# Optimization experiments

Measured on AMD Instinct MI355X. Metric: run time of the kernel, lower is better.

The kernel has to match this reference:

```python
import jax, jax.numpy as jnp
import numpy as np

EPS = 1e-5  # BatchNorm eps; BN applied in eval mode with running_mean=0, running_var=1


def conv1x1(x, w, b=None):
    # x: [B,C,H,W], w: [O,C] -> [B,O,H,W]
    y = jnp.einsum('bchw,oc->bohw', x, w)
    if b is not None:
        y = y + b[None, :, None, None]
    return y


def bn_eval(x, gamma, beta):
    # running_mean=0, running_var=1
    scale = gamma / jnp.sqrt(1.0 + EPS)
    return x * scale[None, :, None, None] + beta[None, :, None, None]


def glnl_forward(x, mask, wt_nl, bt_nl, wp_nl, bp_nl, wt_l, bt_l, wp_l, bp_l,
                 wg_nl, bg_nl, wg_l, bg_l, wW, bW, gW, betaW, wWl, gWl, betaWl):
    B, C, H, W = x.shape
    I = wt_nl.shape[0]
    N = H * W

    # non-local branch score [B,N,N]
    th_nl = conv1x1(x, wt_nl, bt_nl).reshape(B, I, N)
    ph_nl = conv1x1(x, wp_nl, bp_nl).reshape(B, I, N)
    score_nl = jax.nn.softmax(jnp.einsum('bin,bim->bnm', th_nl, ph_nl), axis=-1)

    # local branch: mask-gated projections, score [B,N,N]
    m = mask.reshape(B, 1, N)
    th_l = conv1x1(x, wt_l, bt_l).reshape(B, I, N) * m
    ph_l = conv1x1(x, wp_l, bp_l).reshape(B, I, N) * m
    score_l = jax.nn.softmax(jnp.einsum('bin,bim->bnm', th_l, ph_l), axis=-1)

    # value projections [B,I,N]
    g_nl = conv1x1(x, wg_nl, bg_nl).reshape(B, I, N)
    g_l = conv1x1(x, wg_l, bg_l).reshape(B, I, N)

    # attention aggregation -> [B,I,H,W]
    y_nl = jnp.einsum('bnm,bim->bin', score_nl, g_nl).reshape(B, I, H, W)
    y_l = jnp.einsum('bnm,bim->bin', score_l, g_l).reshape(B, I, H, W)

    # W_local: conv1x1 (no bias) -> ReLU -> BN
    y_l = bn_eval(jax.nn.relu(conv1x1(y_l, wWl)), gWl, betaWl)

    y = y_nl + y_l
    # W: conv1x1 -> ReLU -> BN, then residual
    W_y = bn_eval(jax.nn.relu(conv1x1(y, wW, bW)), gW, betaW)
    return W_y + x


def setup_inputs() -> dict:
    key = jax.random.key(0)
    ks = jax.random.split(key, 20)
    B, C, I, H, W = 4, 128, 64, 64, 64
    s = 0.02
    inp = {
        'x': jax.random.normal(ks[0], (B, C, H, W), jnp.float32),
        'mask': (jax.random.uniform(ks[1], (B, 1, H, W)) > 0.5).astype(jnp.float32),
        'wt_nl': jax.random.normal(ks[2], (I, C)) * s, 'bt_nl': jnp.zeros((I,)),
        'wp_nl': jax.random.normal(ks[3], (I, C)) * s, 'bp_nl': jnp.zeros((I,)),
        'wt_l': jax.random.normal(ks[4], (I, C)) * s, 'bt_l': jnp.zeros((I,)),
        'wp_l': jax.random.normal(ks[5], (I, C)) * s, 'bp_l': jnp.zeros((I,)),
        'wg_nl': jax.random.normal(ks[6], (I, C)) * s, 'bg_nl': jnp.zeros((I,)),
        'wg_l': jax.random.normal(ks[7], (I, C)) * s, 'bg_l': jnp.zeros((I,)),
        'wW': jax.random.normal(ks[8], (C, I)) * s, 'bW': jnp.zeros((C,)),
        'gW': jnp.ones((C,)), 'betaW': jnp.zeros((C,)),
        'wWl': jax.random.normal(ks[9], (I, I)) * s,
        'gWl': jnp.ones((I,)), 'betaWl': jnp.zeros((I,)),
    }
    return inp


def reference(x, mask, wt_nl, bt_nl, wp_nl, bp_nl, wt_l, bt_l, wp_l, bp_l,
              wg_nl, bg_nl, wg_l, bg_l, wW, bW, gW, betaW, wWl, gWl, betaWl):
    return glnl_forward(x, mask, wt_nl, bt_nl, wp_nl, bp_nl, wt_l, bt_l, wp_l, bp_l,
                        wg_nl, bg_nl, wg_l, bg_l, wW, bW, gW, betaW, wWl, gWl, betaWl)
```

## Files before the change

### kernel.cpp

```cpp
#include <hip/hip_runtime.h>

typedef unsigned short u16;
typedef __attribute__((ext_vector_type(8))) short short8;
typedef __attribute__((ext_vector_type(4))) float floatx4;

#define MFMA16(a, b, c) __builtin_amdgcn_mfma_f32_16x16x32_bf16((a), (b), (c), 0, 0, 0)

#define SZ_P ((size_t)4 * 64 * 4096)

__device__ __forceinline__ float bf2f(u16 u) {
    union { unsigned int i; float f; } v; v.i = ((unsigned int)u) << 16; return v.f;
}
__device__ __forceinline__ u16 f2bf(float f) {
    union { float f; unsigned int i; } v; v.f = f;
    unsigned int r = v.i + 0x7fffu + ((v.i >> 16) & 1u);
    return (u16)(r >> 16);
}
__device__ __forceinline__ unsigned int pk2(float a, float b) {
    union { float f; unsigned int u; } x, y; x.f = a; y.f = b;
    return (x.u >> 16) | (y.u & 0xffff0000u);
}

__global__ __launch_bounds__(256) void k_prep_w(
    const float* __restrict__ w0, const float* __restrict__ w1,
    const float* __restrict__ w2, const float* __restrict__ w3,
    const float* __restrict__ w4, const float* __restrict__ w5,
    const float* __restrict__ wWl, const float* __restrict__ wW,
    u16* __restrict__ wbf)
{
    const int idx = blockIdx.x * 256 + threadIdx.x;
    float v;
    if (idx < 49152) {
        const int j = idx >> 13, off = idx & 8191;
        const float* s = (j == 0) ? w0 : (j == 1) ? w1 : (j == 2) ? w2
                       : (j == 3) ? w3 : (j == 4) ? w4 : w5;
        v = s[off];
    } else if (idx < 53248) {
        v = wWl[idx - 49152];
    } else {
        v = wW[idx - 53248];
    }
    wbf[idx] = f2bf(v);
}

__global__ __launch_bounds__(256) void k_proj(
    const float* __restrict__ x, const float* __restrict__ mask,
    const u16* __restrict__ wbf,
    const float* __restrict__ bq0f, const float* __restrict__ bk0f,
    const float* __restrict__ bv0f,
    const float* __restrict__ bq1f, const float* __restrict__ bk1f,
    const float* __restrict__ bv1f,
    u16* __restrict__ q0, u16* __restrict__ k0, u16* __restrict__ v0,
    u16* __restrict__ q1, u16* __restrict__ k1, u16* __restrict__ v1)
{
    __shared__ __align__(16) u16 xt_s[64 * 136];
    const int n0 = blockIdx.x * 64, b = blockIdx.y;
    const int br = blockIdx.z >> 1, half = blockIdx.z & 1;
    const u16* wq = wbf + br * 24576;
    const u16* wk = wq + 8192;
    const u16* wv = wk + 8192;
    const float* bq = br ? bq1f : bq0f;
    const float* bk = br ? bk1f : bk0f;
    const float* bv = br ? bv1f : bv0f;
    u16* q = br ? q1 : q0;  u16* k = br ? k1 : k0;  u16* v = br ? v1 : v0;

    const int t = threadIdx.x, w = t >> 6, lane = t & 63;
    const int quad = lane >> 4, l15 = lane & 15;
    const float* xb = x + ((size_t)b << 19);

    for (int idx = t; idx < 8192; idx += 256) {
        const int c = idx >> 6, n = idx & 63;
        xt_s[n * 136 + c] = f2bf(xb[((size_t)c << 12) + n0 + n]);
    }
    __syncthreads();

    short8 ax[4];
#pragma unroll
    for (int cc = 0; cc < 4; ++cc)
        ax[cc] = *(const short8*)&xt_s[(w * 16 + l15) * 136 + quad * 8 + cc * 32];

    float mv[4] = {1.f, 1.f, 1.f, 1.f};
    if (br) {
#pragma unroll
        for (int r = 0; r < 4; ++r)
            mv[r] = mask[((size_t)b << 12) + n0 + w * 16 + quad * 4 + r];
    }

#pragma unroll
    for (int qk = 0; qk < 2; ++qk) {
        const u16* wsel = qk ? wk : wq;
        const float* bb = qk ? bk : bq;
        u16* o = qk ? k : q;
#pragma unroll
        for (int nsh = 0; nsh < 2; ++nsh) {
            const int ns = half * 2 + nsh;
            floatx4 acc = {0.f, 0.f, 0.f, 0.f};
            const u16* wp = wsel + (ns * 16 + l15) * 128 + quad * 8;
#pragma unroll
            for (int cc = 0; cc < 4; ++cc)
                acc = MFMA16(ax[cc], *(const short8*)(wp + cc * 32), acc);
            const float bias_i = bb[ns * 16 + l15];
#pragma unroll
            for (int r = 0; r < 4; ++r) {
                const float val = (acc[r] + bias_i) * mv[r];
                o[((size_t)b << 18) + (size_t)(n0 + w * 16 + quad * 4 + r) * 64
                  + ns * 16 + l15] = f2bf(val);
            }
        }
    }

    short8 aw[4];
#pragma unroll
    for (int cc = 0; cc < 4; ++cc)
        aw[cc] = *(const short8*)(wv + (w * 16 + l15) * 128 + quad * 8 + cc * 32);
    float bvr[4];
#pragma unroll
    for (int r = 0; r < 4; ++r) bvr[r] = bv[w * 16 + quad * 4 + r];
#pragma unroll
    for (int nsh = 0; nsh < 2; ++nsh) {
        const int ns = half * 2 + nsh;
        floatx4 acc = {0.f, 0.f, 0.f, 0.f};
#pragma unroll
        for (int cc = 0; cc < 4; ++cc)
            acc = MFMA16(aw[cc],
                *(const short8*)&xt_s[(ns * 16 + l15) * 136 + quad * 8 + cc * 32], acc);
#pragma unroll
        for (int r = 0; r < 4; ++r) {
            v[((size_t)b << 18) + ((size_t)(w * 16 + quad * 4 + r) << 12)
              + n0 + ns * 16 + l15] = f2bf(acc[r] + bvr[r]);
        }
    }
}

__global__ __launch_bounds__(256) void k_flash(
    const u16* __restrict__ Q0, const u16* __restrict__ K0,
    const u16* __restrict__ V0,
    const u16* __restrict__ Q1, const u16* __restrict__ K1,
    const u16* __restrict__ V1,
    u16* __restrict__ num, float* __restrict__ den)
{
    __shared__ __align__(16) u16 kt_s[2][64 * 72];
    __shared__ __align__(16) u16 vt_s[2][64 * 72];
    __shared__ __align__(16) u16 p_s[4 * 32 * 72];

    const int flat = blockIdx.x;
    const int g = flat & 15, tile = flat >> 4;
    const int b = g >> 2, z = g & 3;
    const int br = z >> 1, sp = z & 1;
    const int qb = tile * 128;
    const size_t base = ((size_t)b << 18);
    const u16* Q = (br ? Q1 : Q0) + base;
    const u16* K = (br ? K1 : K0) + base;
    const u16* V = (br ? V1 : V0) + base;
    u16* numo = num + (size_t)z * SZ_P + base;
    float* deno = den + z * 16384 + b * 4096;

    const int t = threadIdx.x, w = t >> 6, lane = t & 63;
    const int quad = lane >> 4, l15 = lane & 15;
    const int pw = w * 32 * 72;

    const int r0 = t >> 3, r1 = (t + 256) >> 3, cg8 = (t & 7) * 8;
    const u16* Kp0 = K + (size_t)r0 * 64 + cg8;
    const u16* Kp1 = K + (size_t)r1 * 64 + cg8;
    const u16* Vp0 = V + ((size_t)r0 << 12) + cg8;
    const u16* Vp1 = V + ((size_t)r1 << 12) + cg8;
    const int lk0 = r0 * 72 + cg8, lk1 = r1 * 72 + cg8;

    short8 aq[2][2];
#pragma unroll
    for (int t2 = 0; t2 < 2; ++t2)
#pragma unroll
        for (int s = 0; s < 2; ++s)
            aq[t2][s] = *(const short8*)(Q + (size_t)(qb + w * 32 + t2 * 16 + l15) * 64
                                         + s * 32 + quad * 8);

    const short8 ones8 = {0x3F80, 0x3F80, 0x3F80, 0x3F80, 0x3F80, 0x3F80, 0x3F80, 0x3F80};

    floatx4 oacc[4][2];
#pragma unroll
    for (int it = 0; it < 4; ++it)
#pragma unroll
        for (int t2 = 0; t2 < 2; ++t2) oacc[it][t2] = (floatx4){0.f, 0.f, 0.f, 0.f};
    floatx4 lacc[2] = {{0.f, 0.f, 0.f, 0.f}, {0.f, 0.f, 0.f, 0.f}};

    const int roff = tile & 31;
    const int m_beg = sp * 2048;

    {
        const int m0 = m_beg + (roff << 6);
        *(short8*)&kt_s[0][lk0] = *(const short8*)(Kp0 + (size_t)m0 * 64);
        *(short8*)&kt_s[0][lk1] = *(const short8*)(Kp1 + (size_t)m0 * 64);
        *(short8*)&vt_s[0][lk0] = *(const short8*)(Vp0 + m0);
        *(short8*)&vt_s[0][lk1] = *(const short8*)(Vp1 + m0);
    }

    for (int j = 0; j < 32; ++j) {
        const int cur = j & 1;
        const int mn = m_beg + (((roff + j + 1) & 31) << 6);
        short8 pk0v = *(const short8*)(Kp0 + (size_t)mn * 64);
        short8 pk1v = *(const short8*)(Kp1 + (size_t)mn * 64);
        short8 pv0v = *(const short8*)(Vp0 + mn);
        short8 pv1v = *(const short8*)(Vp1 + mn);
        __syncthreads();

#pragma unroll
        for (int mt = 0; mt < 4; ++mt) {
            const u16* kp = &kt_s[cur][(mt * 16 + l15) * 72 + quad * 8];
            const short8 ka0 = *(const short8*)kp;
            const short8 ka1 = *(const short8*)(kp + 32);
#pragma unroll
            for (int t2 = 0; t2 < 2; ++t2) {
                floatx4 acc = {0.f, 0.f, 0.f, 0.f};
                acc = MFMA16(ka0, aq[t2][0], acc);
                acc = MFMA16(ka1, aq[t2][1], acc);
                const float e0 = __expf(acc[0]), e1 = __expf(acc[1]);
                const float e2 = __expf(acc[2]), e3 = __expf(acc[3]);
                *(uint2*)&p_s[pw + (t2 * 16 + l15) * 72 + mt * 16 + quad * 4] =
                    make_uint2(pk2(e0, e1), pk2(e2, e3));
            }
        }

        short8 pb2[2][2];
#pragma unroll
        for (int t2 = 0; t2 < 2; ++t2)
#pragma unroll
            for (int s = 0; s < 2; ++s)
                pb2[t2][s] = *(const short8*)&p_s[pw + (t2 * 16 + l15) * 72 + s * 32 + quad * 8];
#pragma unroll
        for (int it = 0; it < 4; ++it) {
            const u16* vp = &vt_s[cur][(it * 16 + l15) * 72 + quad * 8];
            const short8 va0 = *(const short8*)vp;
            const short8 va1 = *(const short8*)(vp + 32);
#pragma unroll
            for (int t2 = 0; t2 < 2; ++t2) {
                oacc[it][t2] = MFMA16(va0, pb2[t2][0], oacc[it][t2]);
                oacc[it][t2] = MFMA16(va1, pb2[t2][1], oacc[it][t2]);
            }
        }
#pragma unroll
        for (int t2 = 0; t2 < 2; ++t2) {
            lacc[t2] = MFMA16(ones8, pb2[t2][0], lacc[t2]);
            lacc[t2] = MFMA16(ones8, pb2[t2][1], lacc[t2]);
        }

        *(short8*)&kt_s[cur ^ 1][lk0] = pk0v;
        *(short8*)&kt_s[cur ^ 1][lk1] = pk1v;
        *(short8*)&vt_s[cur ^ 1][lk0] = pv0v;
        *(short8*)&vt_s[cur ^ 1][lk1] = pv1v;
    }

    if (quad == 0) {
#pragma unroll
        for (int t2 = 0; t2 < 2; ++t2)
            deno[qb + w * 32 + t2 * 16 + l15] = lacc[t2][0];
    }

#pragma unroll
    for (int it = 0; it < 4; ++it)
#pragma unroll
        for (int t2 = 0; t2 < 2; ++t2) {
            *(uint2*)&p_s[pw + (t2 * 16 + l15) * 72 + it * 16 + quad * 4] =
                make_uint2(pk2(oacc[it][t2][0], oacc[it][t2][1]),
                           pk2(oacc[it][t2][2], oacc[it][t2][3]));
        }
    __syncthreads();
#pragma unroll
    for (int ch = t; ch < 1024; ch += 256) {
        const int row = ch >> 3, cg = ch & 7;
        *(short8*)(numo + (size_t)(qb + row) * 64 + cg * 8) =
            *(const short8*)&p_s[(row >> 5) * 2304 + (row & 31) * 72 + cg * 8];
    }
}

__global__ __launch_bounds__(256) void k_epi(
    const u16* __restrict__ num, const float* __restrict__ den,
    const u16* __restrict__ wbf,
    const float* __restrict__ gWl, const float* __restrict__ betaWl,
    const float* __restrict__ bW, const float* __restrict__ gW,
    const float* __restrict__ betaW,
    const float* __restrict__ x, float* __restrict__ out)
{
    __shared__ __align__(16) u16 yl_s[16 * 72];
    __shared__ __align__(16) u16 ynl_s[16 * 72];
    __shared__ __align__(16) u16 yy_s[16 * 72];
    const int b = blockIdx.y, n0 = blockIdx.x * 16;
    const int t = threadIdx.x, w = t >> 6, lane = t & 63;
    const int quad = lane >> 4, l15 = lane & 15;
    const size_t ybase = ((size_t)b << 18) + (size_t)n0 * 64;

    if (t < 128) {
        const int row = t >> 3, cg = t & 7;
        const float dn = den[b * 4096 + n0 + row] + den[16384 + b * 4096 + n0 + row];
        const float dl = den[32768 + b * 4096 + n0 + row] + den[49152 + b * 4096 + n0 + row];
        const float inl = 1.0f / dn, ilo = 1.0f / dl;
        const short8 a0 = *(const short8*)(num + ybase + row * 64 + cg * 8);
        const short8 a1 = *(const short8*)(num + SZ_P + ybase + row * 64 + cg * 8);
        const short8 c0 = *(const short8*)(num + 2 * SZ_P + ybase + row * 64 + cg * 8);
        const short8 c1 = *(const short8*)(num + 3 * SZ_P + ybase + row * 64 + cg * 8);
        short8 ynl8, yl8;
#pragma unroll
        for (int j = 0; j < 8; ++j) {
            ynl8[j] = (short)f2bf((bf2f((u16)a0[j]) + bf2f((u16)a1[j])) * inl);
            yl8[j]  = (short)f2bf((bf2f((u16)c0[j]) + bf2f((u16)c1[j])) * ilo);
        }
        *(short8*)&ynl_s[row * 72 + cg * 8] = ynl8;
        *(short8*)&yl_s[row * 72 + cg * 8] = yl8;
    }
    __syncthreads();
    const float rsq = rsqrtf(1.0f + 1e-5f);
    const u16* wblW = wbf + 49152;
    const u16* wbW  = wbf + 53248;

    {
        const short8 a0 = *(const short8*)(wblW + (w * 16 + l15) * 64 + quad * 8);
        const short8 a1 = *(const short8*)(wblW + (w * 16 + l15) * 64 + 32 + quad * 8);
        float sc[4], bt[4];
#pragma unroll
        for (int r = 0; r < 4; ++r) {
            const int io = w * 16 + quad * 4 + r;
            sc[r] = gWl[io] * rsq;
            bt[r] = betaWl[io];
        }
        floatx4 acc = {0.f, 0.f, 0.f, 0.f};
        const u16* bp_ = &yl_s[l15 * 72 + quad * 8];
        acc = MFMA16(a0, *(const short8*)bp_, acc);
        acc = MFMA16(a1, *(const short8*)(bp_ + 32), acc);
#pragma unroll
        for (int r = 0; r < 4; ++r) {
            const int io = w * 16 + quad * 4 + r;
            float val = fmaxf(acc[r], 0.f) * sc[r] + bt[r];
            val += bf2f(ynl_s[l15 * 72 + io]);
            yy_s[l15 * 72 + io] = f2bf(val);
        }
    }
    __syncthreads();

#pragma unroll
    for (int rb = 0; rb < 2; ++rb) {
        const int c0 = rb * 64 + w * 16;
        const short8 a0 = *(const short8*)(wbW + (c0 + l15) * 64 + quad * 8);
        const short8 a1 = *(const short8*)(wbW + (c0 + l15) * 64 + 32 + quad * 8);
        float bs[4], sc[4], bt[4];
#pragma unroll
        for (int r = 0; r < 4; ++r) {
            const int c = c0 + quad * 4 + r;
            bs[r] = bW[c];
            sc[r] = gW[c] * rsq;
            bt[r] = betaW[c];
        }
        floatx4 acc = {0.f, 0.f, 0.f, 0.f};
        const u16* bp_ = &yy_s[l15 * 72 + quad * 8];
        acc = MFMA16(a0, *(const short8*)bp_, acc);
        acc = MFMA16(a1, *(const short8*)(bp_ + 32), acc);
#pragma unroll
        for (int r = 0; r < 4; ++r) {
            const int c = c0 + quad * 4 + r;
            float val = fmaxf(acc[r] + bs[r], 0.f) * sc[r] + bt[r];
            const size_t xi = ((size_t)b << 19) + ((size_t)c << 12) + n0 + l15;
            out[xi] = val + x[xi];
        }
    }
}

extern "C" void kernel_launch(void* const* d_in, const int* in_sizes, int n_in,
                              void* d_out, int out_size, void* d_ws, size_t ws_size,
                              hipStream_t stream) {
    const float* x      = (const float*)d_in[0];
    const float* mask   = (const float*)d_in[1];
    const float* wt_nl  = (const float*)d_in[2];  const float* bt_nl = (const float*)d_in[3];
    const float* wp_nl  = (const float*)d_in[4];  const float* bp_nl = (const float*)d_in[5];
    const float* wt_l   = (const float*)d_in[6];  const float* bt_l  = (const float*)d_in[7];
    const float* wp_l   = (const float*)d_in[8];  const float* bp_l  = (const float*)d_in[9];
    const float* wg_nl  = (const float*)d_in[10]; const float* bg_nl = (const float*)d_in[11];
    const float* wg_l   = (const float*)d_in[12]; const float* bg_l  = (const float*)d_in[13];
    const float* wW     = (const float*)d_in[14]; const float* bW    = (const float*)d_in[15];
    const float* gW     = (const float*)d_in[16]; const float* betaW = (const float*)d_in[17];
    const float* wWl    = (const float*)d_in[18]; const float* gWl   = (const float*)d_in[19];
    const float* betaWl = (const float*)d_in[20];

    u16* ws  = (u16*)d_ws;
    u16* wbf = ws;
    u16* q0  = wbf + 61440;
    u16* k0  = q0 + SZ_P;
    u16* v0  = k0 + SZ_P;
    u16* q1  = v0 + SZ_P;
    u16* k1  = q1 + SZ_P;
    u16* v1  = k1 + SZ_P;
    u16* num = v1 + SZ_P;
    float* den = (float*)(num + 4 * SZ_P);

    k_prep_w<<<dim3(240), 256, 0, stream>>>(wt_nl, wp_nl, wg_nl,
                                            wt_l, wp_l, wg_l, wWl, wW, wbf);
    k_proj<<<dim3(64, 4, 4), 256, 0, stream>>>(x, mask, wbf,
        bt_nl, bp_nl, bg_nl, bt_l, bp_l, bg_l,
        q0, k0, v0, q1, k1, v1);
    k_flash<<<dim3(512), 256, 0, stream>>>(q0, k0, v0, q1, k1, v1, num, den);
    k_epi<<<dim3(256, 4), 256, 0, stream>>>(num, den, wbf, gWl, betaWl,
                                            bW, gW, betaW, x, (float*)d_out);
}
```

Before: 180.6 us.

## Fuse all stages into one persistent kernel with global atomic barriers

Merges the weight-prep, projection, flash-attention and epilogue kernels into one 512-block kernel. The stages are separated by software grid barriers built on atomic counters, which are reset with a memset before each launch. Work is remapped per stage: projection blocks now cover all four output subtiles, and epilogue blocks handle 32 positions. The aim is to remove the launch gaps between kernels, at the cost of barrier spin overhead and relying on all 512 blocks being resident at once.

```diff
diff --git a/kernel.cpp b/kernel.cpp
--- a/kernel.cpp
+++ b/kernel.cpp
@@ -21,343 +21,355 @@
     return (x.u >> 16) | (y.u & 0xffff0000u);
 }
 
-__global__ __launch_bounds__(256) void k_prep_w(
-    const float* __restrict__ w0, const float* __restrict__ w1,
-    const float* __restrict__ w2, const float* __restrict__ w3,
-    const float* __restrict__ w4, const float* __restrict__ w5,
-    const float* __restrict__ wWl, const float* __restrict__ wW,
-    u16* __restrict__ wbf)
+__device__ __forceinline__ void gbar(unsigned int* ctr, unsigned int target) {
+    __syncthreads();
+    __threadfence();
+    if (threadIdx.x == 0) {
+        atomicAdd(ctr, 1u);
+        while (atomicAdd(ctr, 0u) < target) __builtin_amdgcn_s_sleep(8);
+    }
+    __syncthreads();
+    __threadfence();
+}
+
+__global__ __launch_bounds__(256) void k_mega(
+    const float* __restrict__ x, const float* __restrict__ mask,
+    const float* __restrict__ wt_nl, const float* __restrict__ bt_nl,
+    const float* __restrict__ wp_nl, const float* __restrict__ bp_nl,
+    const float* __restrict__ wt_l,  const float* __restrict__ bt_l,
+    const float* __restrict__ wp_l,  const float* __restrict__ bp_l,
+    const float* __restrict__ wg_nl, const float* __restrict__ bg_nl,
+    const float* __restrict__ wg_l,  const float* __restrict__ bg_l,
+    const float* __restrict__ wW,  const float* __restrict__ bW,
+    const float* __restrict__ gW,  const float* __restrict__ betaW,
+    const float* __restrict__ wWl, const float* __restrict__ gWl,
+    const float* __restrict__ betaWl,
+    float* __restrict__ out,
+    u16* __restrict__ wbf,
+    u16* __restrict__ q0, u16* __restrict__ k0, u16* __restrict__ v0,
+    u16* __restrict__ q1, u16* __restrict__ k1, u16* __restrict__ v1,
+    u16* __restrict__ num, float* __restrict__ den,
+    unsigned int* __restrict__ bar)
 {
-    const int idx = blockIdx.x * 256 + threadIdx.x;
-    float v;
-    if (idx < 49152) {
-        const int j = idx >> 13, off = idx & 8191;
-        const float* s = (j == 0) ? w0 : (j == 1) ? w1 : (j == 2) ? w2
-                       : (j == 3) ? w3 : (j == 4) ? w4 : w5;
-        v = s[off];
-    } else if (idx < 53248) {
-        v = wWl[idx - 49152];
-    } else {
-        v = wW[idx - 53248];
-    }
-    wbf[idx] = f2bf(v);
-}
-
-__global__ __launch_bounds__(256) void k_proj(
-    const float* __restrict__ x, const float* __restrict__ mask,
-    const u16* __restrict__ wbf,
-    const float* __restrict__ bq0f, const float* __restrict__ bk0f,
-    const float* __restrict__ bv0f,
-    const float* __restrict__ bq1f, const float* __restrict__ bk1f,
-    const float* __restrict__ bv1f,
-    u16* __restrict__ q0, u16* __restrict__ k0, u16* __restrict__ v0,
-    u16* __restrict__ q1, u16* __restrict__ k1, u16* __restrict__ v1)
-{
-    __shared__ __align__(16) u16 xt_s[64 * 136];
-    const int n0 = blockIdx.x * 64, b = blockIdx.y;
-    const int br = blockIdx.z >> 1, half = blockIdx.z & 1;
-    const u16* wq = wbf + br * 24576;
-    const u16* wk = wq + 8192;
-    const u16* wv = wk + 8192;
-    const float* bq = br ? bq1f : bq0f;
-    const float* bk = br ? bk1f : bk0f;
-    const float* bv = br ? bv1f : bv0f;
-    u16* q = br ? q1 : q0;  u16* k = br ? k1 : k0;  u16* v = br ? v1 : v0;
-
+    __shared__ __align__(16) u16 smem[27648];
+    const int flat = blockIdx.x;
     const int t = threadIdx.x, w = t >> 6, lane = t & 63;
     const int quad = lane >> 4, l15 = lane & 15;
-    const float* xb = x + ((size_t)b << 19);
-
-    for (int idx = t; idx < 8192; idx += 256) {
-        const int c = idx >> 6, n = idx & 63;
-        xt_s[n * 136 + c] = f2bf(xb[((size_t)c << 12) + n0 + n]);
+
+    {
+        const int idx = flat * 256 + t;
+        if (idx < 61440) {
+            float v;
+            if (idx < 49152) {
+                const int j = idx >> 13, off = idx & 8191;
+                const float* s = (j == 0) ? wt_nl : (j == 1) ? wp_nl : (j == 2) ? wg_nl
+                               : (j == 3) ? wt_l : (j == 4) ? wp_l : wg_l;
+                v = s[off];
+            } else if (idx < 53248) {
+                v = wWl[idx - 49152];
+            } else {
+                v = wW[idx - 53248];
+            }
+            wbf[idx] = f2bf(v);
+        }
     }
-    __syncthreads();
-
-    short8 ax[4];
-#pragma unroll
-    for (int cc = 0; cc < 4; ++cc)
-        ax[cc] = *(const short8*)&xt_s[(w * 16 + l15) * 136 + quad * 8 + cc * 32];
-
-    float mv[4] = {1.f, 1.f, 1.f, 1.f};
-    if (br) {
-#pragma unroll
-        for (int r = 0; r < 4; ++r)
-            mv[r] = mask[((size_t)b << 12) + n0 + w * 16 + quad * 4 + r];
+    gbar(bar, 512);
+
+    {
+        u16* xt_s = smem;
+        const int br = flat & 1, b = (flat >> 1) & 3, n0 = (flat >> 3) * 64;
+        const u16* wq = wbf + br * 24576;
+        const u16* wk = wq + 8192;
+        const u16* wv = wk + 8192;
+        const float* bq = br ? bt_l : bt_nl;
+        const float* bk = br ? bp_l : bp_nl;
+        const float* bv = br ? bg_l : bg_nl;
+        u16* q = br ? q1 : q0;  u16* k = br ? k1 : k0;  u16* v = br ? v1 : v0;
+        const float* xb = x + ((size_t)b << 19);
+
+        for (int idx = t; idx < 8192; idx += 256) {
+            const int c = idx >> 6, n = idx & 63;
+            xt_s[n * 136 + c] = f2bf(xb[((size_t)c << 12) + n0 + n]);
+        }
+        __syncthreads();
+
+        short8 ax[4];
+#pragma unroll
+        for (int cc = 0; cc < 4; ++cc)
+            ax[cc] = *(const short8*)&xt_s[(w * 16 + l15) * 136 + quad * 8 + cc * 32];
+
+        float mv[4] = {1.f, 1.f, 1.f, 1.f};
+        if (br) {
+#pragma unroll
+            for (int r = 0; r < 4; ++r)
+                mv[r] = mask[((size_t)b << 12) + n0 + w * 16 + quad * 4 + r];
+        }
+
+#pragma unroll
+        for (int qk = 0; qk < 2; ++qk) {
+            const u16* wsel = qk ? wk : wq;
+            const float* bb = qk ? bk : bq;
+            u16* o = qk ? k : q;
+#pragma unroll
+            for (int ns = 0; ns < 4; ++ns) {
+                floatx4 acc = {0.f, 0.f, 0.f, 0.f};
+                const u16* wp = wsel + (ns * 16 + l15) * 128 + quad * 8;
+#pragma unroll
+                for (int cc = 0; cc < 4; ++cc)
+                    acc = MFMA16(ax[cc], *(const short8*)(wp + cc * 32), acc);
+                const float bias_i = bb[ns * 16 + l15];
+#pragma unroll
+                for (int r = 0; r < 4; ++r) {
+                    const float val = (acc[r] + bias_i) * mv[r];
+                    o[((size_t)b << 18) + (size_t)(n0 + w * 16 + quad * 4 + r) * 64
+                      + ns * 16 + l15] = f2bf(val);
+                }
+            }
+        }
+
+        short8 aw[4];
+#pragma unroll
+        for (int cc = 0; cc < 4; ++cc)
+            aw[cc] = *(const short8*)(wv + (w * 16 + l15) * 128 + quad * 8 + cc * 32);
+        float bvr[4];
+#pragma unroll
+        for (int r = 0; r < 4; ++r) bvr[r] = bv[w * 16 + quad * 4 + r];
+#pragma unroll
+        for (int ns = 0; ns < 4; ++ns) {
+            floatx4 acc = {0.f, 0.f, 0.f, 0.f};
+#pragma unroll
+            for (int cc = 0; cc < 4; ++cc)
+                acc = MFMA16(aw[cc],
+                    *(const short8*)&xt_s[(ns * 16 + l15) * 136 + quad * 8 + cc * 32], acc);
+#pragma unroll
+            for (int r = 0; r < 4; ++r) {
+                v[((size_t)b << 18) + ((size_t)(w * 16 + quad * 4 + r) << 12)
+                  + n0 + ns * 16 + l15] = f2bf(acc[r] + bvr[r]);
+            }
+        }
     }
-
-#pragma unroll
-    for (int qk = 0; qk < 2; ++qk) {
-        const u16* wsel = qk ? wk : wq;
-        const float* bb = qk ? bk : bq;
-        u16* o = qk ? k : q;
-#pragma unroll
-        for (int nsh = 0; nsh < 2; ++nsh) {
-            const int ns = half * 2 + nsh;
-            floatx4 acc = {0.f, 0.f, 0.f, 0.f};
-            const u16* wp = wsel + (ns * 16 + l15) * 128 + quad * 8;
-#pragma unroll
-            for (int cc = 0; cc < 4; ++cc)
-                acc = MFMA16(ax[cc], *(const short8*)(wp + cc * 32), acc);
-            const float bias_i = bb[ns * 16 + l15];
+    gbar(bar + 4, 512);
+
+    {
+        u16* kt_sb = smem;
+        u16* vt_sb = smem + 9216;
+        u16* p_s   = smem + 18432;
+
+        const int g = flat & 15, tile = flat >> 4;
+        const int b = g >> 2, z = g & 3;
+        const int br = z >> 1, sp = z & 1;
+        const int qb = tile * 128;
+        const size_t base = ((size_t)b << 18);
+        const u16* Q = (br ? q1 : q0) + base;
+        const u16* K = (br ? k1 : k0) + base;
+        const u16* V = (br ? v1 : v0) + base;
+        u16* numo = num + (size_t)z * SZ_P + base;
+        float* deno = den + z * 16384 + b * 4096;
+
+        const int pw = w * 32 * 72;
+        const int r0 = t >> 3, r1 = (t + 256) >> 3, cg8 = (t & 7) * 8;
+        const u16* Kp0 = K + (size_t)r0 * 64 + cg8;
+        const u16* Kp1 = K + (size_t)r1 * 64 + cg8;
+        const u16* Vp0 = V + ((size_t)r0 << 12) + cg8;
+        const u16* Vp1 = V + ((size_t)r1 << 12) + cg8;
+        const int lk0 = r0 * 72 + cg8, lk1 = r1 * 72 + cg8;
+
+        short8 aq[2][2];
+#pragma unroll
+        for (int t2 = 0; t2 < 2; ++t2)
+#pragma unroll
+            for (int s = 0; s < 2; ++s)
+                aq[t2][s] = *(const short8*)(Q + (size_t)(qb + w * 32 + t2 * 16 + l15) * 64
+                                             + s * 32 + quad * 8);
+
+        const short8 ones8 = {0x3F80, 0x3F80, 0x3F80, 0x3F80,
+                              0x3F80, 0x3F80, 0x3F80, 0x3F80};
+        floatx4 oacc[4][2];
+#pragma unroll
+        for (int it = 0; it < 4; ++it)
+#pragma unroll
+            for (int t2 = 0; t2 < 2; ++t2) oacc[it][t2] = (floatx4){0.f, 0.f, 0.f, 0.f};
+        floatx4 lacc[2] = {{0.f, 0.f, 0.f, 0.f}, {0.f, 0.f, 0.f, 0.f}};
+
+        const int roff = tile & 31;
+        const int m_beg = sp * 2048;
+
+        {
+            const int m0 = m_beg + (roff << 6);
+            *(short8*)&kt_sb[lk0] = *(const short8*)(Kp0 + (size_t)m0 * 64);
+            *(short8*)&kt_sb[lk1] = *(const short8*)(Kp1 + (size_t)m0 * 64);
+            *(short8*)&vt_sb[lk0] = *(const short8*)(Vp0 + m0);
+            *(short8*)&vt_sb[lk1] = *(const short8*)(Vp1 + m0);
+        }
+
+        for (int j = 0; j < 32; ++j) {
+            const int cur = j & 1;
+            u16* ktc = kt_sb + cur * 4608;
+            u16* vtc = vt_sb + cur * 4608;
+            u16* ktn = kt_sb + (cur ^ 1) * 4608;
+            u16* vtn = vt_sb + (cur ^ 1) * 4608;
+            const int mn = m_beg + (((roff + j + 1) & 31) << 6);
+            short8 pk0v = *(const short8*)(Kp0 + (size_t)mn * 64);
+            short8 pk1v = *(const short8*)(Kp1 + (size_t)mn * 64);
+            short8 pv0v = *(const short8*)(Vp0 + mn);
+            short8 pv1v = *(const short8*)(Vp1 + mn);
+            __syncthreads();
+
+#pragma unroll
+            for (int mt = 0; mt < 4; ++mt) {
+                const u16* kp = &ktc[(mt * 16 + l15) * 72 + quad * 8];
+                const short8 ka0 = *(const short8*)kp;
+                const short8 ka1 = *(const short8*)(kp + 32);
+#pragma unroll
+                for (int t2 = 0; t2 < 2; ++t2) {
+                    floatx4 acc = {0.f, 0.f, 0.f, 0.f};
+                    acc = MFMA16(ka0, aq[t2][0], acc);
+                    acc = MFMA16(ka1, aq[t2][1], acc);
+                    const float e0 = __expf(acc[0]), e1 = __expf(acc[1]);
+                    const float e2 = __expf(acc[2]), e3 = __expf(acc[3]);
+                    *(uint2*)&p_s[pw + (t2 * 16 + l15) * 72 + mt * 16 + quad * 4] =
+                        make_uint2(pk2(e0, e1), pk2(e2, e3));
+                }
+            }
+
+            short8 pb2[2][2];
+#pragma unroll
+            for (int t2 = 0; t2 < 2; ++t2)
+#pragma unroll
+                for (int s = 0; s < 2; ++s)
+                    pb2[t2][s] = *(const short8*)&p_s[pw + (t2 * 16 + l15) * 72 + s * 32 + quad * 8];
+#pragma unroll
+            for (int it = 0; it < 4; ++it) {
+                const u16* vp = &vtc[(it * 16 + l15) * 72 + quad * 8];
+                const short8 va0 = *(const short8*)vp;
+                const short8 va1 = *(const short8*)(vp + 32);
+#pragma unroll
+                for (int t2 = 0; t2 < 2; ++t2) {
+                    oacc[it][t2] = MFMA16(va0, pb2[t2][0], oacc[it][t2]);
+                    oacc[it][t2] = MFMA16(va1, pb2[t2][1], oacc[it][t2]);
+                }
+            }
+#pragma unroll
+            for (int t2 = 0; t2 < 2; ++t2) {
+                lacc[t2] = MFMA16(ones8, pb2[t2][0], lacc[t2]);
+                lacc[t2] = MFMA16(ones8, pb2[t2][1], lacc[t2]);
+            }
+
+            *(short8*)&ktn[lk0] = pk0v;
+            *(short8*)&ktn[lk1] = pk1v;
+            *(short8*)&vtn[lk0] = pv0v;
+            *(short8*)&vtn[lk1] = pv1v;
+        }
+
+        if (quad == 0) {
+#pragma unroll
+            for (int t2 = 0; t2 < 2; ++t2)
+                deno[qb + w * 32 + t2 * 16 + l15] = lacc[t2][0];
+        }
+
+#pragma unroll
+        for (int it = 0; it < 4; ++it)
+#pragma unroll
+            for (int t2 = 0; t2 < 2; ++t2) {
+                *(uint2*)&p_s[pw + (t2 * 16 + l15) * 72 + it * 16 + quad * 4] =
+                    make_uint2(pk2(oacc[it][t2][0], oacc[it][t2][1]),
+                               pk2(oacc[it][t2][2], oacc[it][t2][3]));
+            }
+        __syncthreads();
+#pragma unroll
+        for (int ch = t; ch < 1024; ch += 256) {
+            const int row = ch >> 3, cg = ch & 7;
+            *(short8*)(numo + (size_t)(qb + row) * 64 + cg * 8) =
+                *(const short8*)&p_s[(row >> 5) * 2304 + (row & 31) * 72 + cg * 8];
+        }
+    }
+    gbar(bar + 8, 512);
+
+    {
+        u16* yl_s  = smem;
+        u16* ynl_s = smem + 2304;
+        u16* yy_s  = smem + 4608;
+        const int b = flat & 3, n0 = (flat >> 2) * 32;
+        const size_t ybase = ((size_t)b << 18) + (size_t)n0 * 64;
+
+        {
+            const int row = t >> 3, cg = t & 7;
+            const float dn = den[b * 4096 + n0 + row] + den[16384 + b * 4096 + n0 + row];
+            const float dl = den[32768 + b * 4096 + n0 + row] + den[49152 + b * 4096 + n0 + row];
+            const float inl = 1.0f / dn, ilo = 1.0f / dl;
+            const short8 a0 = *(const short8*)(num + ybase + row * 64 + cg * 8);
+            const short8 a1 = *(const short8*)(num + SZ_P + ybase + row * 64 + cg * 8);
+            const short8 c0 = *(const short8*)(num + 2 * SZ_P + ybase + row * 64 + cg * 8);
+            const short8 c1 = *(const short8*)(num + 3 * SZ_P + ybase + row * 64 + cg * 8);
+            short8 ynl8, yl8;
+#pragma unroll
+            for (int j = 0; j < 8; ++j) {
+                ynl8[j] = (short)f2bf((bf2f((u16)a0[j]) + bf2f((u16)a1[j])) * inl);
+                yl8[j]  = (short)f2bf((bf2f((u16)c0[j]) + bf2f((u16)c1[j])) * ilo);
+            }
+            *(short8*)&ynl_s[row * 72 + cg * 8] = ynl8;
+            *(short8*)&yl_s[row * 72 + cg * 8] = yl8;
+        }
+        __syncthreads();
+        const float rsq = rsqrtf(1.0f + 1e-5f);
+        const u16* wblW = wbf + 49152;
+        const u16* wbW  = wbf + 53248;
+
+        {
+            const short8 a0 = *(const short8*)(wblW + (w * 16 + l15) * 64 + quad * 8);
+            const short8 a1 = *(const short8*)(wblW + (w * 16 + l15) * 64 + 32 + quad * 8);
+            float sc[4], bt[4];
 #pragma unroll
             for (int r = 0; r < 4; ++r) {
-                const float val = (acc[r] + bias_i) * mv[r];
-                o[((size_t)b << 18) + (size_t)(n0 + w * 16 + quad * 4 + r) * 64
-                  + ns * 16 + l15] = f2bf(val);
-            }
-        }
-    }
-
-    short8 aw[4];
-#pragma unroll
-    for (int cc = 0; cc < 4; ++cc)
-        aw[cc] = *(const short8*)(wv + (w * 16 + l15) * 128 + quad * 8 + cc * 32);
-    float bvr[4];
-#pragma unroll
-    for (int r = 0; r < 4; ++r) bvr[r] = bv[w * 16 + quad * 4 + r];
-#pragma unroll
-    for (int nsh = 0; nsh < 2; ++nsh) {
-        const int ns = half * 2 + nsh;
-        floatx4 acc = {0.f, 0.f, 0.f, 0.f};
-#pragma unroll
-        for (int cc = 0; cc < 4; ++cc)
-            acc = MFMA16(aw[cc],
-                *(const short8*)&xt_s[(ns * 16 + l15) * 136 + quad * 8 + cc * 32], acc);
-#pragma unroll
-        for (int r = 0; r < 4; ++r) {
-            v[((size_t)b << 18) + ((size_t)(w * 16 + quad * 4 + r) << 12)
-              + n0 + ns * 16 + l15] = f2bf(acc[r] + bvr[r]);
-        }
-    }
-}
-
-__global__ __launch_bounds__(256) void k_flash(
-    const u16* __restrict__ Q0, const u16* __restrict__ K0,
-    const u16* __restrict__ V0,
-    const u16* __restrict__ Q1, const u16* __restrict__ K1,
-    const u16* __restrict__ V1,
-    u16* __restrict__ num, float* __restrict__ den)
-{
-    __shared__ __align__(16) u16 kt_s[2][64 * 72];
-    __shared__ __align__(16) u16 vt_s[2][64 * 72];
-    __shared__ __align__(16) u16 p_s[4 * 32 * 72];
-
-    const int flat = blockIdx.x;
-    const int g = flat & 15, tile = flat >> 4;
-    const int b = g >> 2, z = g & 3;
-    const int br = z >> 1, sp = z & 1;
-    const int qb = tile * 128;
-    const size_t base = ((size_t)b << 18);
-    const u16* Q = (br ? Q1 : Q0) + base;
-    const u16* K = (br ? K1 : K0) + base;
-    const u16* V = (br ? V1 : V0) + base;
-    u16* numo = num + (size_t)z * SZ_P + base;
-    float* deno = den + z * 16384 + b * 4096;
-
-    const int t = threadIdx.x, w = t >> 6, lane = t & 63;
-    const int quad = lane >> 4, l15 = lane & 15;
-    const int pw = w * 32 * 72;
-
-    const int r0 = t >> 3, r1 = (t + 256) >> 3, cg8 = (t & 7) * 8;
-    const u16* Kp0 = K + (size_t)r0 * 64 + cg8;
-    const u16* Kp1 = K + (size_t)r1 * 64 + cg8;
-    const u16* Vp0 = V + ((size_t)r0 << 12) + cg8;
-    const u16* Vp1 = V + ((size_t)r1 << 12) + cg8;
-    const int lk0 = r0 * 72 + cg8, lk1 = r1 * 72 + cg8;
-
-    short8 aq[2][2];
-#pragma unroll
-    for (int t2 = 0; t2 < 2; ++t2)
-#pragma unroll
-        for (int s = 0; s < 2; ++s)
-            aq[t2][s] = *(const short8*)(Q + (size_t)(qb + w * 32 + t2 * 16 + l15) * 64
-                                         + s * 32 + quad * 8);
-
-    const short8 ones8 = {0x3F80, 0x3F80, 0x3F80, 0x3F80, 0x3F80, 0x3F80, 0x3F80, 0x3F80};
-
-    floatx4 oacc[4][2];
-#pragma unroll
-    for (int it = 0; it < 4; ++it)
-#pragma unroll
-        for (int t2 = 0; t2 < 2; ++t2) oacc[it][t2] = (floatx4){0.f, 0.f, 0.f, 0.f};
-    floatx4 lacc[2] = {{0.f, 0.f, 0.f, 0.f}, {0.f, 0.f, 0.f, 0.f}};
-
-    const int roff = tile & 31;
-    const int m_beg = sp * 2048;
-
-    {
-        const int m0 = m_beg + (roff << 6);
-        *(short8*)&kt_s[0][lk0] = *(const short8*)(Kp0 + (size_t)m0 * 64);
-        *(short8*)&kt_s[0][lk1] = *(const short8*)(Kp1 + (size_t)m0 * 64);
-        *(short8*)&vt_s[0][lk0] = *(const short8*)(Vp0 + m0);
-        *(short8*)&vt_s[0][lk1] = *(const short8*)(Vp1 + m0);
-    }
-
-    for (int j = 0; j < 32; ++j) {
-        const int cur = j & 1;
-        const int mn = m_beg + (((roff + j + 1) & 31) << 6);
-        short8 pk0v = *(const short8*)(Kp0 + (size_t)mn * 64);
-        short8 pk1v = *(const short8*)(Kp1 + (size_t)mn * 64);
-        short8 pv0v = *(const short8*)(Vp0 + mn);
-        short8 pv1v = *(const short8*)(Vp1 + mn);
+                const int io = w * 16 + quad * 4 + r;
+                sc[r] = gWl[io] * rsq;
+                bt[r] = betaWl[io];
+            }
+#pragma unroll
+            for (int ns = 0; ns < 2; ++ns) {
+                floatx4 acc = {0.f, 0.f, 0.f, 0.f};
+                const u16* bp_ = &yl_s[(ns * 16 + l15) * 72 + quad * 8];
+                acc = MFMA16(a0, *(const short8*)bp_, acc);
+                acc = MFMA16(a1, *(const short8*)(bp_ + 32), acc);
+#pragma unroll
+                for (int r = 0; r < 4; ++r) {
+                    const int io = w * 16 + quad * 4 + r;
+                    float val = fmaxf(acc[r], 0.f) * sc[r] + bt[r];
+                    val += bf2f(ynl_s[(ns * 16 + l15) * 72 + io]);
+                    yy_s[(ns * 16 + l15) * 72 + io] = f2bf(val);
+                }
+            }
+        }
         __syncthreads();
 
 #pragma unroll
-        for (int mt = 0; mt < 4; ++mt) {
-            const u16* kp = &kt_s[cur][(mt * 16 + l15) * 72 + quad * 8];
-            const short8 ka0 = *(const short8*)kp;
-            const short8 ka1 = *(const short8*)(kp + 32);
-#pragma unroll
-            for (int t2 = 0; t2 < 2; ++t2) {
+        for (int rb = 0; rb < 2; ++rb) {
+            const int c0 = rb * 64 + w * 16;
+            const short8 a0 = *(const short8*)(wbW + (c0 + l15) * 64 + quad * 8);
+            const short8 a1 = *(const short8*)(wbW + (c0 + l15) * 64 + 32 + quad * 8);
+            float bs[4], sc[4], bt[4];
+#pragma unroll
+            for (int r = 0; r < 4; ++r) {
+                const int c = c0 + quad * 4 + r;
+                bs[r] = bW[c];
+                sc[r] = gW[c] * rsq;
+                bt[r] = betaW[c];
+            }
+#pragma unroll
+            for (int ns = 0; ns < 2; ++ns) {
                 floatx4 acc = {0.f, 0.f, 0.f, 0.f};
-                acc = MFMA16(ka0, aq[t2][0], acc);
-                acc = MFMA16(ka1, aq[t2][1], acc);
-                const float e0 = __expf(acc[0]), e1 = __expf(acc[1]);
-                const float e2 = __expf(acc[2]), e3 = __expf(acc[3]);
-                *(uint2*)&p_s[pw + (t2 * 16 + l15) * 72 + mt * 16 + quad * 4] =
-                    make_uint2(pk2(e0, e1), pk2(e2, e3));
-            }
-        }
-
-        short8 pb2[2][2];
-#pragma unroll
-        for (int t2 = 0; t2 < 2; ++t2)
-#pragma unroll
-            for (int s = 0; s < 2; ++s)
-                pb2[t2][s] = *(const short8*)&p_s[pw + (t2 * 16 + l15) * 72 + s * 32 + quad * 8];
-#pragma unroll
-        for (int it = 0; it < 4; ++it) {
-            const u16* vp = &vt_s[cur][(it * 16 + l15) * 72 + quad * 8];
-            const short8 va0 = *(const short8*)vp;
-            const short8 va1 = *(const short8*)(vp + 32);
-#pragma unroll
-            for (int t2 = 0; t2 < 2; ++t2) {
-                oacc[it][t2] = MFMA16(va0, pb2[t2][0], oacc[it][t2]);
-                oacc[it][t2] = MFMA16(va1, pb2[t2][1], oacc[it][t2]);
-            }
-        }
-#pragma unroll
-        for (int t2 = 0; t2 < 2; ++t2) {
-            lacc[t2] = MFMA16(ones8, pb2[t2][0], lacc[t2]);
-            lacc[t2] = MFMA16(ones8, pb2[t2][1], lacc[t2]);
-        }
-
-        *(short8*)&kt_s[cur ^ 1][lk0] = pk0v;
-        *(short8*)&kt_s[cur ^ 1][lk1] = pk1v;
-        *(short8*)&vt_s[cur ^ 1][lk0] = pv0v;
-        *(short8*)&vt_s[cur ^ 1][lk1] = pv1v;
-    }
-
-    if (quad == 0) {
-#pragma unroll
-        for (int t2 = 0; t2 < 2; ++t2)
-            deno[qb + w * 32 + t2 * 16 + l15] = lacc[t2][0];
-    }
-
-#pragma unroll
-    for (int it = 0; it < 4; ++it)
-#pragma unroll
-        for (int t2 = 0; t2 < 2; ++t2) {
-            *(uint2*)&p_s[pw + (t2 * 16 + l15) * 72 + it * 16 + quad * 4] =
-                make_uint2(pk2(oacc[it][t2][0], oacc[it][t2][1]),
-                           pk2(oacc[it][t2][2], oacc[it][t2][3]));
-        }
-    __syncthreads();
-#pragma unroll
-    for (int ch = t; ch < 1024; ch += 256) {
-        const int row = ch >> 3, cg = ch & 7;
-        *(short8*)(numo + (size_t)(qb + row) * 64 + cg * 8) =
-            *(const short8*)&p_s[(row >> 5) * 2304 + (row & 31) * 72 + cg * 8];
-    }
-}
-
-__global__ __launch_bounds__(256) void k_epi(
-    const u16* __restrict__ num, const float* __restrict__ den,
-    const u16* __restrict__ wbf,
-    const float* __restrict__ gWl, const float* __restrict__ betaWl,
-    const float* __restrict__ bW, const float* __restrict__ gW,
-    const float* __restrict__ betaW,
-    const float* __restrict__ x, float* __restrict__ out)
-{
-    __shared__ __align__(16) u16 yl_s[16 * 72];
-    __shared__ __align__(16) u16 ynl_s[16 * 72];
-    __shared__ __align__(16) u16 yy_s[16 * 72];
-    const int b = blockIdx.y, n0 = blockIdx.x * 16;
-    const int t = threadIdx.x, w = t >> 6, lane = t & 63;
-    const int quad = lane >> 4, l15 = lane & 15;
-    const size_t ybase = ((size_t)b << 18) + (size_t)n0 * 64;
-
-    if (t < 128) {
-        const int row = t >> 3, cg = t & 7;
-        const float dn = den[b * 4096 + n0 + row] + den[16384 + b * 4096 + n0 + row];
-        const float dl = den[32768 + b * 4096 + n0 + row] + den[49152 + b * 4096 + n0 + row];
-        const float inl = 1.0f / dn, ilo = 1.0f / dl;
-        const short8 a0 = *(const short8*)(num + ybase + row * 64 + cg * 8);
-        const short8 a1 = *(const short8*)(num + SZ_P + ybase + row * 64 + cg * 8);
-        const short8 c0 = *(const short8*)(num + 2 * SZ_P + ybase + row * 64 + cg * 8);
-        const short8 c1 = *(const short8*)(num + 3 * SZ_P + ybase + row * 64 + cg * 8);
-        short8 ynl8, yl8;
-#pragma unroll
-        for (int j = 0; j < 8; ++j) {
-            ynl8[j] = (short)f2bf((bf2f((u16)a0[j]) + bf2f((u16)a1[j])) * inl);
-            yl8[j]  = (short)f2bf((bf2f((u16)c0[j]) + bf2f((u16)c1[j])) * ilo);
-        }
-        *(short8*)&ynl_s[row * 72 + cg * 8] = ynl8;
-        *(short8*)&yl_s[row * 72 + cg * 8] = yl8;
-    }
-    __syncthreads();
-    const float rsq = rsqrtf(1.0f + 1e-5f);
-    const u16* wblW = wbf + 49152;
-    const u16* wbW  = wbf + 53248;
-
-    {
-        const short8 a0 = *(const short8*)(wblW + (w * 16 + l15) * 64 + quad * 8);
-        const short8 a1 = *(const short8*)(wblW + (w * 16 + l15) * 64 + 32 + quad * 8);
-        float sc[4], bt[4];
-#pragma unroll
-        for (int r = 0; r < 4; ++r) {
-            const int io = w * 16 + quad * 4 + r;
-            sc[r] = gWl[io] * rsq;
-            bt[r] = betaWl[io];
-        }
-        floatx4 acc = {0.f, 0.f, 0.f, 0.f};
-        const u16* bp_ = &yl_s[l15 * 72 + quad * 8];
-        acc = MFMA16(a0, *(const short8*)bp_, acc);
-        acc = MFMA16(a1, *(const short8*)(bp_ + 32), acc);
-#pragma unroll
-        for (int r = 0; r < 4; ++r) {
-            const int io = w * 16 + quad * 4 + r;
-            float val = fmaxf(acc[r], 0.f) * sc[r] + bt[r];
-            val += bf2f(ynl_s[l15 * 72 + io]);
-            yy_s[l15 * 72 + io] = f2bf(val);
-        }
-    }
-    __syncthreads();
-
-#pragma unroll
-    for (int rb = 0; rb < 2; ++rb) {
-        const int c0 = rb * 64 + w * 16;
-        const short8 a0 = *(const short8*)(wbW + (c0 + l15) * 64 + quad * 8);
-        const short8 a1 = *(const short8*)(wbW + (c0 + l15) * 64 + 32 + quad * 8);
-        float bs[4], sc[4], bt[4];
-#pragma unroll
-        for (int r = 0; r < 4; ++r) {
-            const int c = c0 + quad * 4 + r;
-            bs[r] = bW[c];
-            sc[r] = gW[c] * rsq;
-            bt[r] = betaW[c];
-        }
-        floatx4 acc = {0.f, 0.f, 0.f, 0.f};
-        const u16* bp_ = &yy_s[l15 * 72 + quad * 8];
-        acc = MFMA16(a0, *(const short8*)bp_, acc);
-        acc = MFMA16(a1, *(const short8*)(bp_ + 32), acc);
-#pragma unroll
-        for (int r = 0; r < 4; ++r) {
-            const int c = c0 + quad * 4 + r;
-            float val = fmaxf(acc[r] + bs[r], 0.f) * sc[r] + bt[r];
-            const size_t xi = ((size_t)b << 19) + ((size_t)c << 12) + n0 + l15;
-            out[xi] = val + x[xi];
+                const u16* bp_ = &yy_s[(ns * 16 + l15) * 72 + quad * 8];
+                acc = MFMA16(a0, *(const short8*)bp_, acc);
+                acc = MFMA16(a1, *(const short8*)(bp_ + 32), acc);
+#pragma unroll
+                for (int r = 0; r < 4; ++r) {
+                    const int c = c0 + quad * 4 + r;
+                    float val = fmaxf(acc[r] + bs[r], 0.f) * sc[r] + bt[r];
+                    const size_t xi = ((size_t)b << 19) + ((size_t)c << 12)
+                                    + n0 + ns * 16 + l15;
+                    out[xi] = val + x[xi];
+                }
+            }
         }
     }
 }
@@ -377,6 +389,7 @@
     const float* gW     = (const float*)d_in[16]; const float* betaW = (const float*)d_in[17];
     const float* wWl    = (const float*)d_in[18]; const float* gWl   = (const float*)d_in[19];
     const float* betaWl = (const float*)d_in[20];
+    float* out = (float*)d_out;
 
     u16* ws  = (u16*)d_ws;
     u16* wbf = ws;
@@ -388,13 +401,11 @@
     u16* v1  = k1 + SZ_P;
     u16* num = v1 + SZ_P;
     float* den = (float*)(num + 4 * SZ_P);
-
-    k_prep_w<<<dim3(240), 256, 0, stream>>>(wt_nl, wp_nl, wg_nl,
-                                            wt_l, wp_l, wg_l, wWl, wW, wbf);
-    k_proj<<<dim3(64, 4, 4), 256, 0, stream>>>(x, mask, wbf,
-        bt_nl, bp_nl, bg_nl, bt_l, bp_l, bg_l,
-        q0, k0, v0, q1, k1, v1);
-    k_flash<<<dim3(512), 256, 0, stream>>>(q0, k0, v0, q1, k1, v1, num, den);
-    k_epi<<<dim3(256, 4), 256, 0, stream>>>(num, den, wbf, gWl, betaWl,
-                                            bW, gW, betaW, x, (float*)d_out);
-}
+    unsigned int* bar = (unsigned int*)(den + 4 * 16384);
+
+    hipMemsetAsync((void*)bar, 0, 48, stream);
+    k_mega<<<dim3(512), dim3(256), 0, stream>>>(
+        x, mask, wt_nl, bt_nl, wp_nl, bp_nl, wt_l, bt_l, wp_l, bp_l,
+        wg_nl, bg_nl, wg_l, bg_l, wW, bW, gW, betaW, wWl, gWl, betaWl,
+        out, wbf, q0, k0, v0, q1, k1, v1, num, den, bar);
+}
```

New measurement: 491.3 us. 2.72x slower.

## Drop weight prep kernel, convert weights inline, compute softmax denominators with VALU sums

Applied to the files above, without the earlier changes.

Removes the separate fp32-to-bf16 weight conversion kernel. Projection and epilogue kernels now load fp32 weights and pack them to bf16 in registers. The projection grid is halved so each block computes all four output slices instead of two, which removes the duplicated x transpose into shared memory. In the flash kernel the ones-vector MFMA used for the row-sum denominator is replaced by scalar accumulation of the exponentials plus a cross-lane shuffle reduction, saving MFMA issue slots at the cost of extra VALU adds and fp32 weight loads.

```diff
diff --git a/kernel.cpp b/kernel.cpp
--- a/kernel.cpp
+++ b/kernel.cpp
@@ -16,52 +16,33 @@
     unsigned int r = v.i + 0x7fffu + ((v.i >> 16) & 1u);
     return (u16)(r >> 16);
 }
+__device__ __forceinline__ short8 pack8(const float* __restrict__ p) {
+    short8 r;
+#pragma unroll
+    for (int j = 0; j < 8; ++j) r[j] = (short)f2bf(p[j]);
+    return r;
+}
 __device__ __forceinline__ unsigned int pk2(float a, float b) {
     union { float f; unsigned int u; } x, y; x.f = a; y.f = b;
     return (x.u >> 16) | (y.u & 0xffff0000u);
 }
 
-__global__ __launch_bounds__(256) void k_prep_w(
-    const float* __restrict__ w0, const float* __restrict__ w1,
-    const float* __restrict__ w2, const float* __restrict__ w3,
-    const float* __restrict__ w4, const float* __restrict__ w5,
-    const float* __restrict__ wWl, const float* __restrict__ wW,
-    u16* __restrict__ wbf)
-{
-    const int idx = blockIdx.x * 256 + threadIdx.x;
-    float v;
-    if (idx < 49152) {
-        const int j = idx >> 13, off = idx & 8191;
-        const float* s = (j == 0) ? w0 : (j == 1) ? w1 : (j == 2) ? w2
-                       : (j == 3) ? w3 : (j == 4) ? w4 : w5;
-        v = s[off];
-    } else if (idx < 53248) {
-        v = wWl[idx - 49152];
-    } else {
-        v = wW[idx - 53248];
-    }
-    wbf[idx] = f2bf(v);
-}
-
 __global__ __launch_bounds__(256) void k_proj(
     const float* __restrict__ x, const float* __restrict__ mask,
-    const u16* __restrict__ wbf,
-    const float* __restrict__ bq0f, const float* __restrict__ bk0f,
-    const float* __restrict__ bv0f,
-    const float* __restrict__ bq1f, const float* __restrict__ bk1f,
-    const float* __restrict__ bv1f,
+    const float* __restrict__ wq0, const float* __restrict__ bq0,
+    const float* __restrict__ wk0, const float* __restrict__ bk0,
+    const float* __restrict__ wv0, const float* __restrict__ bv0,
+    const float* __restrict__ wq1, const float* __restrict__ bq1,
+    const float* __restrict__ wk1, const float* __restrict__ bk1,
+    const float* __restrict__ wv1, const float* __restrict__ bv1,
     u16* __restrict__ q0, u16* __restrict__ k0, u16* __restrict__ v0,
     u16* __restrict__ q1, u16* __restrict__ k1, u16* __restrict__ v1)
 {
     __shared__ __align__(16) u16 xt_s[64 * 136];
-    const int n0 = blockIdx.x * 64, b = blockIdx.y;
-    const int br = blockIdx.z >> 1, half = blockIdx.z & 1;
-    const u16* wq = wbf + br * 24576;
-    const u16* wk = wq + 8192;
-    const u16* wv = wk + 8192;
-    const float* bq = br ? bq1f : bq0f;
-    const float* bk = br ? bk1f : bk0f;
-    const float* bv = br ? bv1f : bv0f;
+    const int n0 = blockIdx.x * 64, b = blockIdx.y, br = blockIdx.z;
+    const float* wq = br ? wq1 : wq0;  const float* bq = br ? bq1 : bq0;
+    const float* wk = br ? wk1 : wk0;  const float* bk = br ? bk1 : bk0;
+    const float* wv = br ? wv1 : wv0;  const float* bv = br ? bv1 : bv0;
     u16* q = br ? q1 : q0;  u16* k = br ? k1 : k0;  u16* v = br ? v1 : v0;
 
     const int t = threadIdx.x, w = t >> 6, lane = t & 63;
@@ -88,17 +69,16 @@
 
 #pragma unroll
     for (int qk = 0; qk < 2; ++qk) {
-        const u16* wsel = qk ? wk : wq;
+        const float* wsel = qk ? wk : wq;
         const float* bb = qk ? bk : bq;
         u16* o = qk ? k : q;
 #pragma unroll
-        for (int nsh = 0; nsh < 2; ++nsh) {
-            const int ns = half * 2 + nsh;
+        for (int ns = 0; ns < 4; ++ns) {
             floatx4 acc = {0.f, 0.f, 0.f, 0.f};
-            const u16* wp = wsel + (ns * 16 + l15) * 128 + quad * 8;
+            const float* wp = wsel + (ns * 16 + l15) * 128 + quad * 8;
 #pragma unroll
             for (int cc = 0; cc < 4; ++cc)
-                acc = MFMA16(ax[cc], *(const short8*)(wp + cc * 32), acc);
+                acc = MFMA16(ax[cc], pack8(wp + cc * 32), acc);
             const float bias_i = bb[ns * 16 + l15];
 #pragma unroll
             for (int r = 0; r < 4; ++r) {
@@ -112,13 +92,12 @@
     short8 aw[4];
 #pragma unroll
     for (int cc = 0; cc < 4; ++cc)
-        aw[cc] = *(const short8*)(wv + (w * 16 + l15) * 128 + quad * 8 + cc * 32);
+        aw[cc] = pack8(wv + (w * 16 + l15) * 128 + quad * 8 + cc * 32);
     float bvr[4];
 #pragma unroll
     for (int r = 0; r < 4; ++r) bvr[r] = bv[w * 16 + quad * 4 + r];
 #pragma unroll
-    for (int nsh = 0; nsh < 2; ++nsh) {
-        const int ns = half * 2 + nsh;
+    for (int ns = 0; ns < 4; ++ns) {
         floatx4 acc = {0.f, 0.f, 0.f, 0.f};
 #pragma unroll
         for (int cc = 0; cc < 4; ++cc)
@@ -174,14 +153,12 @@
             aq[t2][s] = *(const short8*)(Q + (size_t)(qb + w * 32 + t2 * 16 + l15) * 64
                                          + s * 32 + quad * 8);
 
-    const short8 ones8 = {0x3F80, 0x3F80, 0x3F80, 0x3F80, 0x3F80, 0x3F80, 0x3F80, 0x3F80};
-
     floatx4 oacc[4][2];
 #pragma unroll
     for (int it = 0; it < 4; ++it)
 #pragma unroll
         for (int t2 = 0; t2 < 2; ++t2) oacc[it][t2] = (floatx4){0.f, 0.f, 0.f, 0.f};
-    floatx4 lacc[2] = {{0.f, 0.f, 0.f, 0.f}, {0.f, 0.f, 0.f, 0.f}};
+    float dacc[2] = {0.f, 0.f};
 
     const int roff = tile & 31;
     const int m_beg = sp * 2048;
@@ -215,6 +192,7 @@
                 acc = MFMA16(ka1, aq[t2][1], acc);
                 const float e0 = __expf(acc[0]), e1 = __expf(acc[1]);
                 const float e2 = __expf(acc[2]), e3 = __expf(acc[3]);
+                dacc[t2] += (e0 + e1) + (e2 + e3);
                 *(uint2*)&p_s[pw + (t2 * 16 + l15) * 72 + mt * 16 + quad * 4] =
                     make_uint2(pk2(e0, e1), pk2(e2, e3));
             }
@@ -237,11 +215,6 @@
                 oacc[it][t2] = MFMA16(va1, pb2[t2][1], oacc[it][t2]);
             }
         }
-#pragma unroll
-        for (int t2 = 0; t2 < 2; ++t2) {
-            lacc[t2] = MFMA16(ones8, pb2[t2][0], lacc[t2]);
-            lacc[t2] = MFMA16(ones8, pb2[t2][1], lacc[t2]);
-        }
 
         *(short8*)&kt_s[cur ^ 1][lk0] = pk0v;
         *(short8*)&kt_s[cur ^ 1][lk1] = pk1v;
@@ -249,10 +222,12 @@
         *(short8*)&vt_s[cur ^ 1][lk1] = pv1v;
     }
 
-    if (quad == 0) {
-#pragma unroll
-        for (int t2 = 0; t2 < 2; ++t2)
-            deno[qb + w * 32 + t2 * 16 + l15] = lacc[t2][0];
+#pragma unroll
+    for (int t2 = 0; t2 < 2; ++t2) {
+        float d = dacc[t2];
+        d += __shfl_xor(d, 16, 64);
+        d += __shfl_xor(d, 32, 64);
+        if (quad == 0) deno[qb + w * 32 + t2 * 16 + l15] = d;
     }
 
 #pragma unroll
@@ -274,10 +249,10 @@
 
 __global__ __launch_bounds__(256) void k_epi(
     const u16* __restrict__ num, const float* __restrict__ den,
-    const u16* __restrict__ wbf,
-    const float* __restrict__ gWl, const float* __restrict__ betaWl,
-    const float* __restrict__ bW, const float* __restrict__ gW,
-    const float* __restrict__ betaW,
+    const float* __restrict__ wWl, const float* __restrict__ gWl,
+    const float* __restrict__ betaWl,
+    const float* __restrict__ wW, const float* __restrict__ bW,
+    const float* __restrict__ gW, const float* __restrict__ betaW,
     const float* __restrict__ x, float* __restrict__ out)
 {
     __shared__ __align__(16) u16 yl_s[16 * 72];
@@ -308,12 +283,10 @@
     }
     __syncthreads();
     const float rsq = rsqrtf(1.0f + 1e-5f);
-    const u16* wblW = wbf + 49152;
-    const u16* wbW  = wbf + 53248;
 
     {
-        const short8 a0 = *(const short8*)(wblW + (w * 16 + l15) * 64 + quad * 8);
-        const short8 a1 = *(const short8*)(wblW + (w * 16 + l15) * 64 + 32 + quad * 8);
+        const short8 a0 = pack8(wWl + (w * 16 + l15) * 64 + quad * 8);
+        const short8 a1 = pack8(wWl + (w * 16 + l15) * 64 + 32 + quad * 8);
         float sc[4], bt[4];
 #pragma unroll
         for (int r = 0; r < 4; ++r) {
@@ -338,8 +311,8 @@
 #pragma unroll
     for (int rb = 0; rb < 2; ++rb) {
         const int c0 = rb * 64 + w * 16;
-        const short8 a0 = *(const short8*)(wbW + (c0 + l15) * 64 + quad * 8);
-        const short8 a1 = *(const short8*)(wbW + (c0 + l15) * 64 + 32 + quad * 8);
+        const short8 a0 = pack8(wW + (c0 + l15) * 64 + quad * 8);
+        const short8 a1 = pack8(wW + (c0 + l15) * 64 + 32 + quad * 8);
         float bs[4], sc[4], bt[4];
 #pragma unroll
         for (int r = 0; r < 4; ++r) {
@@ -379,8 +352,7 @@
     const float* betaWl = (const float*)d_in[20];
 
     u16* ws  = (u16*)d_ws;
-    u16* wbf = ws;
-    u16* q0  = wbf + 61440;
+    u16* q0  = ws;
     u16* k0  = q0 + SZ_P;
     u16* v0  = k0 + SZ_P;
     u16* q1  = v0 + SZ_P;
@@ -389,12 +361,11 @@
     u16* num = v1 + SZ_P;
     float* den = (float*)(num + 4 * SZ_P);
 
-    k_prep_w<<<dim3(240), 256, 0, stream>>>(wt_nl, wp_nl, wg_nl,
-                                            wt_l, wp_l, wg_l, wWl, wW, wbf);
-    k_proj<<<dim3(64, 4, 4), 256, 0, stream>>>(x, mask, wbf,
-        bt_nl, bp_nl, bg_nl, bt_l, bp_l, bg_l,
+    k_proj<<<dim3(64, 4, 2), 256, 0, stream>>>(x, mask,
+        wt_nl, bt_nl, wp_nl, bp_nl, wg_nl, bg_nl,
+        wt_l,  bt_l,  wp_l,  bp_l,  wg_l,  bg_l,
         q0, k0, v0, q1, k1, v1);
     k_flash<<<dim3(512), 256, 0, stream>>>(q0, k0, v0, q1, k1, v1, num, den);
-    k_epi<<<dim3(256, 4), 256, 0, stream>>>(num, den, wbf, gWl, betaWl,
-                                            bW, gW, betaW, x, (float*)d_out);
-}
+    k_epi<<<dim3(256, 4), 256, 0, stream>>>(num, den, wWl, gWl, betaWl,
+                                            wW, bW, gW, betaW, x, (float*)d_out);
+}
```

Measured after the change: 189.7 us. 5.0% more time.
